# Optimization experiments

Hardware: AMD Instinct MI355X
Metric: run time of the kernel (lower is better)

## Reference

```python
import jax, jax.numpy as jnp
import numpy as np

# Model dims (from init_kwargs)
D_MODEL = 1024
D_STATE = 64
D_CONV = 4
EXPAND = 2
HEADDIM = 128
NGROUPS = 1
D_INNER = EXPAND * D_MODEL              # 2048
NHEADS = D_INNER // HEADDIM             # 16
CONV_DIM = D_INNER + 2 * NGROUPS * D_STATE   # 2176
D_IN_PROJ = 2 * D_INNER + 2 * NGROUPS * D_STATE + NHEADS  # 4240
BATCH, SEQLEN = 2, 2048
DT_MIN, DT_MAX, DT_FLOOR = 1e-3, 1e-1, 1e-4
RMS_EPS = 1e-5


def setup_inputs() -> dict:
    key = jax.random.key(0)
    ks = jax.random.split(key, 8)
    u = jax.random.normal(ks[0], (BATCH, SEQLEN, D_MODEL), jnp.float32)
    in_proj_w = jax.random.normal(ks[1], (D_IN_PROJ, D_MODEL), jnp.float32) * 0.02
    conv_w = jax.random.normal(ks[2], (CONV_DIM, 1, D_CONV), jnp.float32) * 0.2
    conv_b = jax.random.normal(ks[3], (CONV_DIM,), jnp.float32) * 0.02
    # dt_bias init: inverse-softplus of dt ~ LogUniform(dt_min, dt_max)
    dt = jnp.exp(jax.random.uniform(ks[4], (NHEADS,)) * (jnp.log(DT_MAX) - jnp.log(DT_MIN)) + jnp.log(DT_MIN))
    dt = jnp.maximum(dt, DT_FLOOR)
    dt_bias = dt + jnp.log(-jnp.expm1(-dt))
    A_log = jnp.log(jax.random.uniform(ks[5], (NHEADS,), minval=1.0, maxval=16.0))
    D_param = jnp.ones((NHEADS,), jnp.float32)
    norm_w = jnp.ones((D_INNER,), jnp.float32)
    out_proj_w = jax.random.normal(ks[6], (D_MODEL, D_INNER), jnp.float32) * 0.02
    return {"u": u, "in_proj_w": in_proj_w, "conv_w": conv_w, "conv_b": conv_b,
            "dt_bias": dt_bias, "A_log": A_log, "D_param": D_param,
            "norm_w": norm_w, "out_proj_w": out_proj_w}


def _mamba2_forward(u, in_proj_w, conv_w, conv_b, dt_bias, A_log, D_param, norm_w, out_proj_w):
    B, L, _ = u.shape
    zxbcdt = jnp.einsum('bld,ed->ble', u, in_proj_w)  # (B, L, D_IN_PROJ)
    z = zxbcdt[..., :D_INNER]
    xBC = zxbcdt[..., D_INNER:D_INNER + CONV_DIM]
    dt = jax.nn.softplus(zxbcdt[..., D_INNER + CONV_DIM:] + dt_bias)  # (B, L, H)

    # Depthwise causal conv1d + SiLU
    xc = jnp.swapaxes(xBC, 1, 2)  # (B, C, L)
    xc = jax.lax.conv_general_dilated(xc, conv_w, window_strides=(1,),
                                      padding=[(D_CONV - 1, 0)],
                                      feature_group_count=CONV_DIM)
    xc = jax.nn.silu(xc + conv_b[None, :, None])
    xBC = jnp.swapaxes(xc, 1, 2)  # (B, L, C)

    x = xBC[..., :D_INNER].reshape(B, L, NHEADS, HEADDIM)
    Bmat = xBC[..., D_INNER:D_INNER + D_STATE]          # (B, L, N), ngroups=1
    Cmat = xBC[..., D_INNER + D_STATE:]                 # (B, L, N)

    A = -jnp.exp(A_log)  # (H,)

    def step(state, inp):
        dt_t, x_t, B_t, C_t = inp  # (B,H), (B,H,P), (B,N), (B,N)
        dA = jnp.exp(dt_t * A)[:, :, None, None]
        state = state * dA + (dt_t[:, :, None, None] * x_t[:, :, :, None]) * B_t[:, None, None, :]
        y_t = jnp.einsum('bhpn,bn->bhp', state, C_t) + D_param[None, :, None] * x_t
        return state, y_t

    state0 = jnp.zeros((B, NHEADS, HEADDIM, D_STATE), u.dtype)
    inputs = (jnp.moveaxis(dt, 1, 0), jnp.moveaxis(x, 1, 0),
              jnp.moveaxis(Bmat, 1, 0), jnp.moveaxis(Cmat, 1, 0))
    _, ys = jax.lax.scan(step, state0, inputs)
    y = jnp.moveaxis(ys, 0, 1).reshape(B, L, D_INNER)

    # RMSNormGated (norm_before_gate=False): gate first, then normalize
    yg = y * jax.nn.silu(z)
    rms = jax.lax.rsqrt(jnp.mean(yg * yg, axis=-1, keepdims=True) + RMS_EPS)
    yn = yg * rms * norm_w

    return jnp.einsum('ble,de->bld', yn, out_proj_w)


def reference(u, in_proj_w, conv_w, conv_b, dt_bias, A_log, D_param, norm_w, out_proj_w):
    return _mamba2_forward(u, in_proj_w, conv_w, conv_b, dt_bias, A_log, D_param, norm_w, out_proj_w)
```

## Files before the change

kernel.cpp:

```cpp
#include <hip/hip_runtime.h>
#include <cstdint>
#include <cstddef>

#define D_MODEL   1024
#define D_STATE   64
#define D_CONV    4
#define HEADDIM   128
#define NHEADS    16
#define D_INNER   2048
#define CONV_DIM  2176
#define D_IN_PROJ 4240
#define NPAD      4352
#define BATCH     2
#define SEQLEN    2048
#define NROWS     (BATCH*SEQLEN)
#define CHUNK     64
#define NCHUNK    (SEQLEN/CHUNK)

using u16   = unsigned short;
using s16x8 = __attribute__((ext_vector_type(8))) short;
using f32x4 = __attribute__((ext_vector_type(4))) float;

__device__ __forceinline__ u16 f2bf(float f) {
    union { float f; unsigned u; } v; v.f = f;
    unsigned r = v.u + 0x7fffu + ((v.u >> 16) & 1u);
    return (u16)(r >> 16);
}
__device__ __forceinline__ float bf2f(u16 x) {
    union { unsigned u; float f; } v; v.u = ((unsigned)x) << 16;
    return v.f;
}

__device__ __forceinline__ void gload16(const u16* g, u16* l) {
    __builtin_amdgcn_global_load_lds(
        (const __attribute__((address_space(1))) unsigned int*)g,
        (__attribute__((address_space(3))) unsigned int*)l, 16, 0, 0);
}

__device__ __forceinline__ void cp8(const float* in, u16* out, int i) {
    const float4* p = (const float4*)(in + (size_t)i * 8);
    float4 a = p[0], b = p[1];
    u16 o[8] = {f2bf(a.x), f2bf(a.y), f2bf(a.z), f2bf(a.w),
                f2bf(b.x), f2bf(b.y), f2bf(b.z), f2bf(b.w)};
    *(uint4*)(out + (size_t)i * 8) = *(const uint4*)o;
}

#define CVT_N0 (NROWS*D_MODEL/8)
#define CVT_N1 (NPAD*128)
#define CVT_N2 (D_MODEL*D_INNER/8)
__global__ __launch_bounds__(256) void cvt_all(
    const float* __restrict__ u, const float* __restrict__ w_in,
    const float* __restrict__ w_out,
    u16* __restrict__ u_bf, u16* __restrict__ w_in_bf, u16* __restrict__ w_out_bf)
{
    int i = blockIdx.x * 256 + threadIdx.x;
    if (i < CVT_N0) {
        cp8(u, u_bf, i);
    } else if (i < CVT_N0 + CVT_N1) {
        int j = i - CVT_N0;
        int row = j >> 7, seg = j & 127;
        u16 o[8] = {0,0,0,0,0,0,0,0};
        if (row < D_IN_PROJ) {
            const float4* p = (const float4*)(w_in + (size_t)row * D_MODEL + seg * 8);
            float4 a = p[0], b = p[1];
            o[0]=f2bf(a.x); o[1]=f2bf(a.y); o[2]=f2bf(a.z); o[3]=f2bf(a.w);
            o[4]=f2bf(b.x); o[5]=f2bf(b.y); o[6]=f2bf(b.z); o[7]=f2bf(b.w);
        }
        *(uint4*)(w_in_bf + (size_t)j * 8) = *(const uint4*)o;
    } else if (i < CVT_N0 + CVT_N1 + CVT_N2) {
        cp8(w_out, w_out_bf, i - CVT_N0 - CVT_N1);
    }
}

#define CPITCH 136
__global__ __launch_bounds__(512) void gemm_in512(
    const u16* __restrict__ A, const u16* __restrict__ B, int K,
    u16* __restrict__ C0, int n1, int ld0,
    u16* __restrict__ C1, int n2, int ld1,
    u16* __restrict__ C2, int n3, int ld2)
{
    __shared__ u16 smem[4 * 128 * 64];

    const int tid  = threadIdx.x;
    const int wid  = tid >> 6;
    const int lane = tid & 63;
    const int wm   = wid >> 2, wn = wid & 3;

    const int gx   = gridDim.x;
    int orig = blockIdx.y * gx + blockIdx.x;
    const int xcd = orig & 7;
    const int loc = orig >> 3;
    const int mt  = (xcd >> 1) * 8  + (loc & 7);
    const int nt  = (xcd & 1) * 17 + (loc >> 3);
    const int m0 = mt * 128, n0 = nt * 128;

    const int lrow = lane >> 3;
    const int lseg = (lane & 7) ^ lrow;
    const u16* gA = A + (size_t)(m0 + lrow) * K + lseg * 8;
    const u16* gB = B + (size_t)(n0 + lrow) * K + lseg * 8;

    f32x4 acc[4][2];
    #pragma unroll
    for (int i = 0; i < 4; ++i)
        #pragma unroll
        for (int j = 0; j < 2; ++j)
            acc[i][j] = (f32x4){0.f, 0.f, 0.f, 0.f};

    const int fr = lane & 15, fq = lane >> 4;
    const int nstep = K >> 6;

    auto stage = [&](int buf, int k0) {
        u16* sAp = smem + buf * 8192;
        u16* sBp = smem + 16384 + buf * 8192;
        #pragma unroll
        for (int i = 0; i < 2; ++i) {
            const int r0 = (i * 8 + wid) * 8;
            gload16(gA + (size_t)r0 * K + k0, sAp + r0 * 64);
            gload16(gB + (size_t)r0 * K + k0, sBp + r0 * 64);
        }
    };

    stage(0, 0);
    int cur = 0;
    for (int step = 0; step < nstep; ++step) {
        if (step + 1 < nstep) {
            stage(cur ^ 1, (step + 1) * 64);
            asm volatile("s_waitcnt vmcnt(4)" ::: "memory");
        } else {
            asm volatile("s_waitcnt vmcnt(0)" ::: "memory");
        }
        __builtin_amdgcn_s_barrier();
        __builtin_amdgcn_sched_barrier(0);

        const u16* sAc = smem + cur * 8192;
        const u16* sBc = smem + 16384 + cur * 8192;
        #pragma unroll
        for (int ks = 0; ks < 2; ++ks) {
            s16x8 bfr[2];
            #pragma unroll
            for (int ni = 0; ni < 2; ++ni) {
                const int row = wn * 32 + ni * 16 + fr;
                const int bo = row * 128 + ((ks * 64 + fq * 16) ^ ((row & 7) << 4));
                bfr[ni] = *(const s16x8*)((const char*)sBc + bo);
            }
            #pragma unroll
            for (int mi = 0; mi < 4; ++mi) {
                const int row = wm * 64 + mi * 16 + fr;
                const int bo = row * 128 + ((ks * 64 + fq * 16) ^ ((row & 7) << 4));
                s16x8 af = *(const s16x8*)((const char*)sAc + bo);
                #pragma unroll
                for (int ni = 0; ni < 2; ++ni)
                    acc[mi][ni] = __builtin_amdgcn_mfma_f32_16x16x32_bf16(
                        af, bfr[ni], acc[mi][ni], 0, 0, 0);
            }
        }

        __builtin_amdgcn_sched_barrier(0);
        __builtin_amdgcn_s_barrier();
        cur ^= 1;
    }
    __builtin_amdgcn_sched_barrier(0);

    u16* sC = smem;
    #pragma unroll
    for (int mi = 0; mi < 4; ++mi) {
        #pragma unroll
        for (int j = 0; j < 4; ++j) {
            const int rl = wm * 64 + mi * 16 + fq * 4 + j;
            #pragma unroll
            for (int ni = 0; ni < 2; ++ni) {
                const int cl = wn * 32 + ni * 16 + fr;
                sC[rl * CPITCH + cl] = f2bf(acc[mi][ni][j]);
            }
        }
    }
    __syncthreads();
    #pragma unroll
    for (int k2 = 0; k2 < 4; ++k2) {
        const int g  = tid + k2 * 512;
        const int rl = g >> 4, cg = g & 15;
        uint4 v = *(const uint4*)&sC[rl * CPITCH + cg * 8];
        const int r = m0 + rl, c = n0 + cg * 8;
        if (c < n1)      *(uint4*)(C0 + (size_t)r * ld0 + c)        = v;
        else if (c < n2) *(uint4*)(C1 + (size_t)r * ld1 + (c - n1)) = v;
        else if (c < n3) *(uint4*)(C2 + (size_t)r * ld2 + (c - n2)) = v;
    }
}

__global__ __launch_bounds__(512) void gemm_out512(
    const u16* __restrict__ A, const u16* __restrict__ B, int K,
    float* __restrict__ C, int N)
{
    __shared__ u16 smem[4 * 128 * 64];

    const int tid  = threadIdx.x;
    const int wid  = tid >> 6;
    const int lane = tid & 63;
    const int wm   = wid >> 2, wn = wid & 3;

    const int gx   = gridDim.x;
    const int nwg  = gx * gridDim.y;
    const int cpx  = nwg >> 3;
    int orig = blockIdx.y * gx + blockIdx.x;
    int wg   = (orig & 7) * cpx + (orig >> 3);
    const int m0 = (wg / gx) * 128, n0 = (wg % gx) * 128;

    const int lrow = lane >> 3;
    const int lseg = (lane & 7) ^ lrow;
    const u16* gA = A + (size_t)(m0 + lrow) * K + lseg * 8;
    const u16* gB = B + (size_t)(n0 + lrow) * K + lseg * 8;

    f32x4 acc[4][2];
    #pragma unroll
    for (int i = 0; i < 4; ++i)
        #pragma unroll
        for (int j = 0; j < 2; ++j)
            acc[i][j] = (f32x4){0.f, 0.f, 0.f, 0.f};

    const int fr = lane & 15, fq = lane >> 4;
    const int nstep = K >> 6;

    auto stage = [&](int buf, int k0) {
        u16* sAp = smem + buf * 8192;
        u16* sBp = smem + 16384 + buf * 8192;
        #pragma unroll
        for (int i = 0; i < 2; ++i) {
            const int r0 = (i * 8 + wid) * 8;
            gload16(gA + (size_t)r0 * K + k0, sAp + r0 * 64);
            gload16(gB + (size_t)r0 * K + k0, sBp + r0 * 64);
        }
    };

    stage(0, 0);
    int cur = 0;
    for (int step = 0; step < nstep; ++step) {
        if (step + 1 < nstep) {
            stage(cur ^ 1, (step + 1) * 64);
            asm volatile("s_waitcnt vmcnt(4)" ::: "memory");
        } else {
            asm volatile("s_waitcnt vmcnt(0)" ::: "memory");
        }
        __builtin_amdgcn_s_barrier();
        __builtin_amdgcn_sched_barrier(0);

        const u16* sAc = smem + cur * 8192;
        const u16* sBc = smem + 16384 + cur * 8192;
        #pragma unroll
        for (int ks = 0; ks < 2; ++ks) {
            s16x8 bfr[2];
            #pragma unroll
            for (int ni = 0; ni < 2; ++ni) {
                const int row = wn * 32 + ni * 16 + fr;
                const int bo = row * 128 + ((ks * 64 + fq * 16) ^ ((row & 7) << 4));
                bfr[ni] = *(const s16x8*)((const char*)sBc + bo);
            }
            #pragma unroll
            for (int mi = 0; mi < 4; ++mi) {
                const int row = wm * 64 + mi * 16 + fr;
                const int bo = row * 128 + ((ks * 64 + fq * 16) ^ ((row & 7) << 4));
                s16x8 af = *(const s16x8*)((const char*)sAc + bo);
                #pragma unroll
                for (int ni = 0; ni < 2; ++ni)
                    acc[mi][ni] = __builtin_amdgcn_mfma_f32_16x16x32_bf16(
                        af, bfr[ni], acc[mi][ni], 0, 0, 0);
            }
        }

        __builtin_amdgcn_sched_barrier(0);
        __builtin_amdgcn_s_barrier();
        cur ^= 1;
    }
    __builtin_amdgcn_sched_barrier(0);

    float* sCf = (float*)smem;
    #pragma unroll
    for (int h2 = 0; h2 < 2; ++h2) {
        if (wm == h2) {
            #pragma unroll
            for (int mi = 0; mi < 4; ++mi)
                #pragma unroll
                for (int j = 0; j < 4; ++j) {
                    const int rl = mi * 16 + fq * 4 + j;
                    #pragma unroll
                    for (int ni = 0; ni < 2; ++ni) {
                        const int cl = wn * 32 + ni * 16 + fr;
                        sCf[rl * 132 + cl] = acc[mi][ni][j];
                    }
                }
        }
        __syncthreads();
        #pragma unroll
        for (int k2 = 0; k2 < 4; ++k2) {
            const int g  = tid + k2 * 512;
            const int rl = g >> 5, cg = g & 31;
            float4 v = *(const float4*)&sCf[rl * 132 + cg * 4];
            *(float4*)(C + (size_t)(m0 + h2 * 64 + rl) * N + n0 + cg * 4) = v;
        }
        __syncthreads();
    }
}

#define NCONV8 (NROWS*(CONV_DIM/8))
__global__ __launch_bounds__(256) void conv_silu_dt(
    const u16* __restrict__ xBC, const float* __restrict__ conv_w,
    const float* __restrict__ conv_b, u16* __restrict__ xconv,
    const u16* __restrict__ dtraw, const float* __restrict__ dt_bias,
    float* __restrict__ dtw)
{
    int idx = blockIdx.x * 256 + threadIdx.x;
    if (idx < NCONV8) {
        int c8  = idx % (CONV_DIM / 8);
        int row = idx / (CONV_DIM / 8);
        int l   = row % SEQLEN;
        int b   = row / SEQLEN;
        int c0  = c8 * 8;
        const u16* src = xBC + (size_t)(b * SEQLEN) * CONV_DIM + c0;

        uint4 z4 = {0u, 0u, 0u, 0u};
        uint4 v3 = *(const uint4*)(src + (size_t)l * CONV_DIM);
        uint4 v2 = (l >= 1) ? *(const uint4*)(src + (size_t)(l-1) * CONV_DIM) : z4;
        uint4 v1 = (l >= 2) ? *(const uint4*)(src + (size_t)(l-2) * CONV_DIM) : z4;
        uint4 v0 = (l >= 3) ? *(const uint4*)(src + (size_t)(l-3) * CONV_DIM) : z4;
        const u16* p0 = (const u16*)&v0; const u16* p1 = (const u16*)&v1;
        const u16* p2 = (const u16*)&v2; const u16* p3 = (const u16*)&v3;

        u16 o[8];
        #pragma unroll
        for (int j = 0; j < 8; ++j) {
            const float4 w4 = *(const float4*)(conv_w + (size_t)(c0 + j) * 4);
            float acc = conv_b[c0 + j]
                      + bf2f(p0[j]) * w4.x + bf2f(p1[j]) * w4.y
                      + bf2f(p2[j]) * w4.z + bf2f(p3[j]) * w4.w;
            o[j] = f2bf(acc / (1.f + expf(-acc)));
        }
        *(uint4*)(xconv + (size_t)row * CONV_DIM + c0) = *(const uint4*)o;
    } else {
        int k = idx - NCONV8;
        if (k < NROWS * NHEADS) {
            int h = k & (NHEADS - 1);
            float v = bf2f(dtraw[k]) + dt_bias[h];
            dtw[k] = (v > 20.f) ? v : log1pf(expf(v));
        }
    }
}

__global__ __launch_bounds__(256) void chunk_state(
    const u16* __restrict__ xconv, const float* __restrict__ dtw,
    const float* __restrict__ A_log, u16* __restrict__ Sbuf,
    float* __restrict__ Tbuf)
{
    const int blk = blockIdx.x;
    const int k  = blk & (NCHUNK-1);
    const int bh = blk >> 5;
    const int b  = bh >> 4, h = bh & 15;
    const int tid = threadIdx.x;
    const int wid = tid >> 6, lane = tid & 63;
    const float A = -expf(A_log[h]);

    __shared__ float sdt[CHUNK], sW[CHUNK], sT;
    __shared__ u16   sWB16[CHUNK * D_STATE];
    __shared__ u16   sX[CHUNK * HEADDIM];

    const int t0 = k * CHUNK;
    const u16* xc = xconv + (size_t)(b*SEQLEN + t0) * CONV_DIM;

    if (tid < CHUNK)
        sdt[tid] = dtw[(size_t)(b*SEQLEN + t0 + tid)*NHEADS + h];
    __syncthreads();
    if (tid < CHUNK) {
        float a = 0.f, pref = 0.f;
        for (int r = 0; r < CHUNK; ++r) {
            a += sdt[r] * A;
            if (r == tid) pref = a;
        }
        sW[tid] = __expf(a - pref) * sdt[tid];
        if (tid == 0) sT = a;
    }
    __syncthreads();

    #pragma unroll
    for (int c = 0; c < 4; ++c) {
        const int r = wid * 16 + c * 4 + (lane >> 4);
        const int seg = lane & 15;
        gload16(xc + (size_t)r * CONV_DIM + h * HEADDIM + seg * 8,
                sX + (wid * 16 + c * 4) * HEADDIM);
    }
    {
        const int s = tid >> 2, nb = tid & 3;
        const float wv = sW[s];
        uint4 b0 = *(const uint4*)(xc + (size_t)s*CONV_DIM + D_INNER + nb*16);
        uint4 b1 = *(const uint4*)(xc + (size_t)s*CONV_DIM + D_INNER + nb*16 + 8);
        const u16* pb0 = (const u16*)&b0; const u16* pb1 = (const u16*)&b1;
        u16 o[16];
        #pragma unroll
        for (int j = 0; j < 8; ++j) {
            o[j]     = f2bf(wv * bf2f(pb0[j]));
            o[8 + j] = f2bf(wv * bf2f(pb1[j]));
        }
        #pragma unroll
        for (int u2 = 0; u2 < 2; ++u2) {
            const int bo = s * 128 + ((nb * 32 + u2 * 16) ^ ((s & 7) << 4));
            *(uint4*)((char*)sWB16 + bo) = *(const uint4*)&o[u2 * 8];
        }
    }
    __syncthreads();

    const int nn = tid >> 4, pp = tid & 15;
    const int p0 = pp * 8, n0 = nn * 4;
    const int base16 = (nn >> 1) << 4;
    const int sub8   = (nn & 1) * 8;
    float acc[4][8];
    #pragma unroll
    for (int i = 0; i < 4; ++i)
        #pragma unroll
        for (int j = 0; j < 8; ++j) acc[i][j] = 0.f;

    for (int sb = 0; sb < CHUNK; sb += 4) {
        #pragma unroll
        for (int si = 0; si < 4; ++si) {
            const int s = sb + si;
            const int bo = s * 128 + ((base16 ^ ((s & 7) << 4)) + sub8);
            uint2 wv2 = *(const uint2*)((const char*)sWB16 + bo);
            const u16* wp = (const u16*)&wv2;
            const float w0f = bf2f(wp[0]), w1f = bf2f(wp[1]);
            const float w2f = bf2f(wp[2]), w3f = bf2f(wp[3]);
            uint4 xv = *(const uint4*)&sX[s * HEADDIM + p0];
            const u16* xp = (const u16*)&xv;
            #pragma unroll
            for (int j = 0; j < 8; ++j) {
                const float xf = bf2f(xp[j]);
                acc[0][j] += w0f * xf;
                acc[1][j] += w1f * xf;
                acc[2][j] += w2f * xf;
                acc[3][j] += w3f * xf;
            }
        }
    }
    u16* So = Sbuf + ((size_t)bh*NCHUNK + k)*(D_STATE*HEADDIM);
    #pragma unroll
    for (int i = 0; i < 4; ++i) {
        u16 o[8];
        #pragma unroll
        for (int j = 0; j < 8; ++j) o[j] = f2bf(acc[i][j]);
        *(uint4*)(So + (size_t)(n0 + i) * HEADDIM + p0) = *(const uint4*)o;
    }
    if (tid == 0) Tbuf[bh*NCHUNK + k] = sT;
}

__global__ __launch_bounds__(256) void chunk_seq_par(u16* __restrict__ Sbuf,
                                                     const float* __restrict__ Tbuf)
{
    const int blk = blockIdx.x;
    const int bh  = blk >> 3;
    const int sub = blk & 7;
    __shared__ float seT[NCHUNK];
    if (threadIdx.x < NCHUNK)
        seT[threadIdx.x] = __expf(Tbuf[bh*NCHUNK + threadIdx.x]);
    __syncthreads();

    const int idx4 = sub * 256 + threadIdx.x;
    u16* base = Sbuf + (size_t)bh*NCHUNK*(D_STATE*HEADDIM) + (size_t)idx4*4;
    float run[4];
    #pragma unroll
    for (int j = 0; j < 4; ++j) run[j] = 0.f;
    for (int k = 0; k < NCHUNK; ++k) {
        u16* p = base + (size_t)k * (D_STATE*HEADDIM);
        uint2 v = *(const uint2*)p;
        const u16* pv = (const u16*)&v;
        const float eT = seT[k];
        u16 o[4];
        #pragma unroll
        for (int j = 0; j < 4; ++j) {
            float tmp = bf2f(pv[j]);
            o[j] = f2bf(run[j]);
            run[j] = run[j] * eT + tmp;
        }
        *(uint2*)p = *(const uint2*)o;
    }
}

__global__ __launch_bounds__(256) void chunk_output(
    const u16* __restrict__ xconv, const float* __restrict__ dtw,
    const float* __restrict__ A_log, const float* __restrict__ D_param,
    const u16* __restrict__ Sbuf, u16* __restrict__ y)
{
    const int blk = blockIdx.x;
    const int k  = blk & (NCHUNK-1);
    const int bh = blk >> 5;
    const int b  = bh >> 4, h = bh & 15;
    const int tid = threadIdx.x;
    const int wid = tid >> 6, lane = tid & 63;
    const float A  = -expf(A_log[h]);
    const float Dp = D_param[h];

    __shared__ u16 sMt16[(CHUNK + D_STATE) * CHUNK];
    __shared__ u16 sX[CHUNK * HEADDIM];
    float* sdt = (float*)sMt16;
    float* sL  = sdt + CHUNK;

    const int t0 = k * CHUNK;
    const u16* xc = xconv + (size_t)(b*SEQLEN + t0) * CONV_DIM;

    if (tid < CHUNK)
        sdt[tid] = dtw[(size_t)(b*SEQLEN + t0 + tid)*NHEADS + h];
    __syncthreads();
    if (tid < CHUNK) {
        float a = 0.f, pref = 0.f;
        for (int r = 0; r < CHUNK; ++r) {
            a += sdt[r] * A;
            if (r == tid) pref = a;
        }
        sL[tid] = pref;
    }
    __syncthreads();

    #pragma unroll
    for (int c = 0; c < 4; ++c) {
        const int r = wid * 16 + c * 4 + (lane >> 4);
        const int seg = lane & 15;
        gload16(xc + (size_t)r * CONV_DIM + h * HEADDIM + seg * 8,
                sX + (wid * 16 + c * 4) * HEADDIM);
    }

    const int fr = lane & 15, fq = lane >> 4;
    float4 sL4 = *(const float4*)&sL[wid * 16 + fq * 4];
    const float Lt[4] = {sL4.x, sL4.y, sL4.z, sL4.w};
    float pre_L[4], pre_dt[4];
    #pragma unroll
    for (int sf = 0; sf < 4; ++sf) {
        const int s_row = sf * 16 + fr;
        pre_L[sf]  = sL[s_row];
        pre_dt[sf] = sdt[s_row];
    }
    const int tM = tid >> 2, nbM = tid & 3;
    const float elM = __expf(sL[tM]);
    __syncthreads();

    {
        const int t_row = wid * 16 + fr;
        s16x8 cfrag[2];
        #pragma unroll
        for (int ks = 0; ks < 2; ++ks)
            cfrag[ks] = *(const s16x8*)(xc + (size_t)t_row*CONV_DIM + D_INNER + D_STATE
                                        + ks*32 + fq*8);

        #pragma unroll
        for (int sf = 0; sf < 4; ++sf) {
            const int s_row = sf * 16 + fr;
            f32x4 g = (f32x4){0.f, 0.f, 0.f, 0.f};
            #pragma unroll
            for (int ks = 0; ks < 2; ++ks) {
                s16x8 bfrag = *(const s16x8*)(xc + (size_t)s_row*CONV_DIM + D_INNER
                                              + ks*32 + fq*8);
                g = __builtin_amdgcn_mfma_f32_16x16x32_bf16(cfrag[ks], bfrag, g, 0, 0, 0);
            }
            const float Ls  = pre_L[sf];
            const float dts = pre_dt[sf];
            u16 o[4];
            #pragma unroll
            for (int r = 0; r < 4; ++r) {
                const int t = wid * 16 + fq * 4 + r;
                const float e = __expf(fminf(Lt[r] - Ls, 0.f)) * dts;
                o[r] = f2bf((s_row <= t) ? g[r] * e : 0.f);
            }
            const int bo2 = s_row * 128 + ((wid * 32 + fq * 8) ^ ((s_row & 7) << 4));
            *(uint2*)((char*)sMt16 + bo2) = *(const uint2*)o;
        }
    }

    {
        uint4 c0 = *(const uint4*)(xc + (size_t)tM*CONV_DIM + D_INNER + D_STATE + nbM*16);
        uint4 c1 = *(const uint4*)(xc + (size_t)tM*CONV_DIM + D_INNER + D_STATE + nbM*16 + 8);
        const u16* pc0 = (const u16*)&c0; const u16* pc1 = (const u16*)&c1;
        #pragma unroll
        for (int j = 0; j < 16; ++j) {
            const int n = nbM * 16 + j;
            const float v = elM * bf2f(j < 8 ? pc0[j] : pc1[j - 8]);
            const int bo2 = (CHUNK + n) * 128 + ((tM * 2) ^ ((n & 7) << 4));
            *(u16*)((char*)sMt16 + bo2) = f2bf(v);
        }
    }
    __syncthreads();

    const int tt = tid >> 4, pp = tid & 15;
    const int p0 = pp * 8;
    float acc[4][8];
    #pragma unroll
    for (int i = 0; i < 4; ++i)
        #pragma unroll
        for (int j = 0; j < 8; ++j) acc[i][j] = 0.f;

    const int smax = tt * 4 + 4;
    for (int sb = 0; sb < smax; sb += 4) {
        #pragma unroll
        for (int si = 0; si < 4; ++si) {
            const int s = sb + si;
            const int bo = s * 128 + ((tt * 8) ^ ((s & 7) << 4));
            uint2 mv = *(const uint2*)((const char*)sMt16 + bo);
            const u16* mp = (const u16*)&mv;
            const float m0f = bf2f(mp[0]), m1f = bf2f(mp[1]);
            const float m2f = bf2f(mp[2]), m3f = bf2f(mp[3]);
            uint4 xv = *(const uint4*)&sX[s * HEADDIM + p0];
            const u16* xp = (const u16*)&xv;
            #pragma unroll
            for (int j = 0; j < 8; ++j) {
                const float xf = bf2f(xp[j]);
                acc[0][j] += m0f * xf;
                acc[1][j] += m1f * xf;
                acc[2][j] += m2f * xf;
                acc[3][j] += m3f * xf;
            }
        }
    }
    const u16* Sinit = Sbuf + ((size_t)bh*NCHUNK + k)*(D_STATE*HEADDIM);
    #pragma unroll 8
    for (int n = 0; n < D_STATE; ++n) {
        const int bo = (CHUNK + n) * 128 + ((tt * 8) ^ ((n & 7) << 4));
        uint2 mv = *(const uint2*)((const char*)sMt16 + bo);
        const u16* mp = (const u16*)&mv;
        const float m0f = bf2f(mp[0]), m1f = bf2f(mp[1]);
        const float m2f = bf2f(mp[2]), m3f = bf2f(mp[3]);
        uint4 sv = *(const uint4*)(Sinit + (size_t)n * HEADDIM + p0);
        const u16* sp = (const u16*)&sv;
        #pragma unroll
        for (int j = 0; j < 8; ++j) {
            const float sf = bf2f(sp[j]);
            acc[0][j] += m0f * sf;
            acc[1][j] += m1f * sf;
            acc[2][j] += m2f * sf;
            acc[3][j] += m3f * sf;
        }
    }
    #pragma unroll
    for (int i = 0; i < 4; ++i) {
        const int t = tt * 4 + i;
        uint4 xv = *(const uint4*)&sX[t * HEADDIM + p0];
        const u16* xp = (const u16*)&xv;
        u16 o[8];
        #pragma unroll
        for (int j = 0; j < 8; ++j)
            o[j] = f2bf(acc[i][j] + Dp * bf2f(xp[j]));
        *(uint4*)(y + ((size_t)(b*SEQLEN + t0 + t))*D_INNER + h*HEADDIM + p0)
            = *(const uint4*)o;
    }
}

__global__ __launch_bounds__(256) void gate_rmsnorm(const u16* __restrict__ z,
                                                    const u16* __restrict__ y,
                                                    const float* __restrict__ norm_w,
                                                    u16* __restrict__ yn)
{
    const int row = blockIdx.x;
    const int tid = threadIdx.x;
    const u16* zr = z + (size_t)row * D_INNER + tid * 8;
    const u16* yr = y + (size_t)row * D_INNER + tid * 8;
    u16*       o  = yn + (size_t)row * D_INNER + tid * 8;

    uint4 zv4 = *(const uint4*)zr;
    uint4 yv4 = *(const uint4*)yr;
    const u16* zp = (const u16*)&zv4;
    const u16* yp = (const u16*)&yv4;

    float vals[8];
    float ss = 0.f;
    #pragma unroll
    for (int j = 0; j < 8; ++j) {
        float zv = bf2f(zp[j]);
        float g  = bf2f(yp[j]) * (zv / (1.f + expf(-zv)));
        vals[j] = g;
        ss += g * g;
    }
    #pragma unroll
    for (int off = 32; off > 0; off >>= 1) ss += __shfl_down(ss, off);
    __shared__ float red[4];
    __shared__ float sscale;
    int wid = tid >> 6, lane = tid & 63;
    if (lane == 0) red[wid] = ss;
    __syncthreads();
    if (tid == 0)
        sscale = rsqrtf((red[0]+red[1]+red[2]+red[3]) / (float)D_INNER + 1e-5f);
    __syncthreads();
    float rms = sscale;
    const float4* nw = (const float4*)(norm_w + tid * 8);
    float4 w0 = nw[0], w1 = nw[1];
    float wv[8] = {w0.x,w0.y,w0.z,w0.w,w1.x,w1.y,w1.z,w1.w};
    u16 ov[8];
    #pragma unroll
    for (int j = 0; j < 8; ++j) ov[j] = f2bf(vals[j] * rms * wv[j]);
    *(uint4*)o = *(const uint4*)ov;
}

extern "C" void kernel_launch(void* const* d_in, const int* in_sizes, int n_in,
                              void* d_out, int out_size, void* d_ws, size_t ws_size,
                              hipStream_t stream)
{
    const float* u          = (const float*)d_in[0];
    const float* in_proj_w  = (const float*)d_in[1];
    const float* conv_w     = (const float*)d_in[2];
    const float* conv_b     = (const float*)d_in[3];
    const float* dt_bias    = (const float*)d_in[4];
    const float* A_log      = (const float*)d_in[5];
    const float* D_param    = (const float*)d_in[6];
    const float* norm_w     = (const float*)d_in[7];
    const float* out_proj_w = (const float*)d_in[8];
    float* out = (float*)d_out;

    char* w = (char*)d_ws;
    u16* z_bf     = (u16*)w;  w += (size_t)NROWS * D_INNER  * 2;
    u16* xBC_bf   = (u16*)w;  w += (size_t)NROWS * CONV_DIM * 2;
    u16* xconv_bf = (u16*)w;  w += (size_t)NROWS * CONV_DIM * 2;
    u16* yb_bf    = (u16*)w;  w += (size_t)NROWS * D_INNER  * 2;
    u16* dtraw_bf = (u16*)w;  w += (size_t)NROWS * NHEADS   * 2;
    float* dtw    = (float*)w; w += (size_t)NROWS * NHEADS  * 4;
    float* Tbuf   = (float*)w; w += (size_t)BATCH*NHEADS*NCHUNK * 4;
    u16* Sbuf     = (u16*)w;  w += (size_t)BATCH*NHEADS*NCHUNK*D_STATE*HEADDIM * 2;
    u16* u_bf     = (u16*)w;  w += (size_t)NROWS * D_MODEL  * 2;
    u16* w_in_bf  = (u16*)w;  w += (size_t)NPAD  * D_MODEL  * 2;
    u16* w_out_bf = (u16*)w;  w += (size_t)D_MODEL * D_INNER * 2;
    u16* yn_bf    = xconv_bf;

    cvt_all<<<(CVT_N0+CVT_N1+CVT_N2 + 255)/256, 256, 0, stream>>>(
        u, in_proj_w, out_proj_w, u_bf, w_in_bf, w_out_bf);

    dim3 g1(NPAD/128, NROWS/128);
    gemm_in512<<<g1, 512, 0, stream>>>(u_bf, w_in_bf, D_MODEL,
                                       z_bf, D_INNER, D_INNER,
                                       xBC_bf, D_INNER + CONV_DIM, CONV_DIM,
                                       dtraw_bf, D_IN_PROJ, NHEADS);

    int ntot = NCONV8 + NROWS * NHEADS;
    conv_silu_dt<<<(ntot + 255) / 256, 256, 0, stream>>>(
        xBC_bf, conv_w, conv_b, xconv_bf, dtraw_bf, dt_bias, dtw);

    chunk_state<<<BATCH*NHEADS*NCHUNK, 256, 0, stream>>>(xconv_bf, dtw, A_log, Sbuf, Tbuf);
    chunk_seq_par<<<BATCH*NHEADS*8, 256, 0, stream>>>(Sbuf, Tbuf);
    chunk_output<<<BATCH*NHEADS*NCHUNK, 256, 0, stream>>>(xconv_bf, dtw, A_log, D_param,
                                                          Sbuf, yb_bf);

    gate_rmsnorm<<<NROWS, 256, 0, stream>>>(z_bf, yb_bf, norm_w, yn_bf);

    dim3 g6(D_MODEL/128, NROWS/128);
    gemm_out512<<<g6, 512, 0, stream>>>(yn_bf, w_out_bf, D_INNER, out, D_MODEL);
}
```

Before: 202.9 us.

## Use MFMA for chunk output intra-chunk and state contributions

Replaces the scalar FMA loops in chunk_output with bf16 MFMA: the masked decay matrix and scaled C are concatenated into one 64x128 A operand, and x and the initial state are transposed into swizzled LDS as the B operand. Results go through an LDS staging buffer so global stores are coalesced. This cuts the FP32 ALU work of the two GEMM-like loops, at the cost of scattered 2-byte transposing LDS writes and an extra synchronisation. The causal-mask skipping that the scalar loop exploited is lost, so the full 64-wide K range is always computed.

```diff
diff --git a/kernel.cpp b/kernel.cpp
--- a/kernel.cpp
+++ b/kernel.cpp
@@ -493,13 +493,17 @@
     const float A  = -expf(A_log[h]);
     const float Dp = D_param[h];
 
-    __shared__ u16 sMt16[(CHUNK + D_STATE) * CHUNK];
-    __shared__ u16 sX[CHUNK * HEADDIM];
-    float* sdt = (float*)sMt16;
+    __shared__ u16 arena[3 * 8192];
+    u16* Mfull = arena;
+    u16* sXT   = arena + 8192;
+    u16* sST   = arena + 16384;
+    u16* eT    = arena + 8192;
+    float* sdt = (float*)Mfull;
     float* sL  = sdt + CHUNK;
 
     const int t0 = k * CHUNK;
     const u16* xc = xconv + (size_t)(b*SEQLEN + t0) * CONV_DIM;
+    const u16* Sinit = Sbuf + ((size_t)bh*NCHUNK + k)*(D_STATE*HEADDIM);
 
     if (tid < CHUNK)
         sdt[tid] = dtw[(size_t)(b*SEQLEN + t0 + tid)*NHEADS + h];
@@ -514,14 +518,6 @@
     }
     __syncthreads();
 
-    #pragma unroll
-    for (int c = 0; c < 4; ++c) {
-        const int r = wid * 16 + c * 4 + (lane >> 4);
-        const int seg = lane & 15;
-        gload16(xc + (size_t)r * CONV_DIM + h * HEADDIM + seg * 8,
-                sX + (wid * 16 + c * 4) * HEADDIM);
-    }
-
     const int fr = lane & 15, fq = lane >> 4;
     float4 sL4 = *(const float4*)&sL[wid * 16 + fq * 4];
     const float Lt[4] = {sL4.x, sL4.y, sL4.z, sL4.w};
@@ -537,6 +533,28 @@
     __syncthreads();
 
     {
+        const int sr = tid >> 2;
+        const int pg = tid & 3;
+        #pragma unroll
+        for (int i = 0; i < 4; ++i) {
+            const int pb = pg * 32 + i * 8;
+            uint4 xv = *(const uint4*)(xc + (size_t)sr * CONV_DIM + h * HEADDIM + pb);
+            const u16* xp = (const u16*)&xv;
+            uint4 sv = *(const uint4*)(Sinit + (size_t)sr * HEADDIM + pb);
+            const u16* sp = (const u16*)&sv;
+            const int cb = sr * 2;
+            const int cbase = (cb & ~15), coff = (cb & 15);
+            #pragma unroll
+            for (int j = 0; j < 8; ++j) {
+                const int p = pb + j;
+                const int bo = p * 128 + (cbase ^ ((p & 7) << 4)) + coff;
+                *(u16*)((char*)sXT + bo) = xp[j];
+                *(u16*)((char*)sST + bo) = sp[j];
+            }
+        }
+    }
+
+    {
         const int t_row = wid * 16 + fr;
         s16x8 cfrag[2];
         #pragma unroll
@@ -556,92 +574,83 @@
             }
             const float Ls  = pre_L[sf];
             const float dts = pre_dt[sf];
-            u16 o[4];
+            const int cb = s_row * 2;
+            const int cbase = (cb & ~15), coff = (cb & 15);
             #pragma unroll
             for (int r = 0; r < 4; ++r) {
                 const int t = wid * 16 + fq * 4 + r;
                 const float e = __expf(fminf(Lt[r] - Ls, 0.f)) * dts;
-                o[r] = f2bf((s_row <= t) ? g[r] * e : 0.f);
-            }
-            const int bo2 = s_row * 128 + ((wid * 32 + fq * 8) ^ ((s_row & 7) << 4));
-            *(uint2*)((char*)sMt16 + bo2) = *(const uint2*)o;
-        }
-    }
-
+                const float val = (s_row <= t) ? g[r] * e : 0.f;
+                const int bo = t * 256 + (cbase ^ ((t & 7) << 4)) + coff;
+                *(u16*)((char*)Mfull + bo) = f2bf(val);
+            }
+        }
+    }
     {
         uint4 c0 = *(const uint4*)(xc + (size_t)tM*CONV_DIM + D_INNER + D_STATE + nbM*16);
         uint4 c1 = *(const uint4*)(xc + (size_t)tM*CONV_DIM + D_INNER + D_STATE + nbM*16 + 8);
         const u16* pc0 = (const u16*)&c0; const u16* pc1 = (const u16*)&c1;
-        #pragma unroll
-        for (int j = 0; j < 16; ++j) {
-            const int n = nbM * 16 + j;
-            const float v = elM * bf2f(j < 8 ? pc0[j] : pc1[j - 8]);
-            const int bo2 = (CHUNK + n) * 128 + ((tM * 2) ^ ((n & 7) << 4));
-            *(u16*)((char*)sMt16 + bo2) = f2bf(v);
-        }
-    }
-    __syncthreads();
-
-    const int tt = tid >> 4, pp = tid & 15;
-    const int p0 = pp * 8;
-    float acc[4][8];
-    #pragma unroll
-    for (int i = 0; i < 4; ++i)
-        #pragma unroll
-        for (int j = 0; j < 8; ++j) acc[i][j] = 0.f;
-
-    const int smax = tt * 4 + 4;
-    for (int sb = 0; sb < smax; sb += 4) {
-        #pragma unroll
-        for (int si = 0; si < 4; ++si) {
-            const int s = sb + si;
-            const int bo = s * 128 + ((tt * 8) ^ ((s & 7) << 4));
-            uint2 mv = *(const uint2*)((const char*)sMt16 + bo);
-            const u16* mp = (const u16*)&mv;
-            const float m0f = bf2f(mp[0]), m1f = bf2f(mp[1]);
-            const float m2f = bf2f(mp[2]), m3f = bf2f(mp[3]);
-            uint4 xv = *(const uint4*)&sX[s * HEADDIM + p0];
-            const u16* xp = (const u16*)&xv;
-            #pragma unroll
-            for (int j = 0; j < 8; ++j) {
-                const float xf = bf2f(xp[j]);
-                acc[0][j] += m0f * xf;
-                acc[1][j] += m1f * xf;
-                acc[2][j] += m2f * xf;
-                acc[3][j] += m3f * xf;
-            }
-        }
-    }
-    const u16* Sinit = Sbuf + ((size_t)bh*NCHUNK + k)*(D_STATE*HEADDIM);
-    #pragma unroll 8
-    for (int n = 0; n < D_STATE; ++n) {
-        const int bo = (CHUNK + n) * 128 + ((tt * 8) ^ ((n & 7) << 4));
-        uint2 mv = *(const uint2*)((const char*)sMt16 + bo);
-        const u16* mp = (const u16*)&mv;
-        const float m0f = bf2f(mp[0]), m1f = bf2f(mp[1]);
-        const float m2f = bf2f(mp[2]), m3f = bf2f(mp[3]);
-        uint4 sv = *(const uint4*)(Sinit + (size_t)n * HEADDIM + p0);
-        const u16* sp = (const u16*)&sv;
-        #pragma unroll
-        for (int j = 0; j < 8; ++j) {
-            const float sf = bf2f(sp[j]);
-            acc[0][j] += m0f * sf;
-            acc[1][j] += m1f * sf;
-            acc[2][j] += m2f * sf;
-            acc[3][j] += m3f * sf;
-        }
-    }
-    #pragma unroll
-    for (int i = 0; i < 4; ++i) {
-        const int t = tt * 4 + i;
-        uint4 xv = *(const uint4*)&sX[t * HEADDIM + p0];
-        const u16* xp = (const u16*)&xv;
-        u16 o[8];
-        #pragma unroll
-        for (int j = 0; j < 8; ++j)
-            o[j] = f2bf(acc[i][j] + Dp * bf2f(xp[j]));
-        *(uint4*)(y + ((size_t)(b*SEQLEN + t0 + t))*D_INNER + h*HEADDIM + p0)
-            = *(const uint4*)o;
+        u16 o[16];
+        #pragma unroll
+        for (int j = 0; j < 16; ++j)
+            o[j] = f2bf(elM * bf2f(j < 8 ? pc0[j] : pc1[j - 8]));
+        #pragma unroll
+        for (int u2 = 0; u2 < 2; ++u2) {
+            const int cb = 128 + nbM * 32 + u2 * 16;
+            const int bo = tM * 256 + (cb ^ ((tM & 7) << 4));
+            *(uint4*)((char*)Mfull + bo) = *(const uint4*)&o[u2 * 8];
+        }
+    }
+    __syncthreads();
+
+    f32x4 accB[8];
+    #pragma unroll
+    for (int i = 0; i < 8; ++i) accB[i] = (f32x4){0.f, 0.f, 0.f, 0.f};
+
+    #pragma unroll
+    for (int ks = 0; ks < 4; ++ks) {
+        const int ta = wid * 16 + fr;
+        const int boA = ta * 256 + ((ks * 64 + fq * 16) ^ ((ta & 7) << 4));
+        s16x8 afr = *(const s16x8*)((const char*)Mfull + boA);
+        const u16* src = (ks < 2) ? sXT : sST;
+        const int cbB = (ks & 1) * 64 + fq * 16;
+        #pragma unroll
+        for (int pt = 0; pt < 8; ++pt) {
+            const int p = pt * 16 + fr;
+            const int boB = p * 128 + (cbB ^ ((p & 7) << 4));
+            s16x8 bfrB = *(const s16x8*)((const char*)src + boB);
+            accB[pt] = __builtin_amdgcn_mfma_f32_16x16x32_bf16(afr, bfrB, accB[pt], 0, 0, 0);
+        }
+    }
+
+    #pragma unroll
+    for (int pt = 0; pt < 8; ++pt) {
+        const int p = pt * 16 + fr;
+        #pragma unroll
+        for (int r = 0; r < 4; ++r) {
+            const int t = wid * 16 + fq * 4 + r;
+            const int cb = t * 2;
+            const int bo = p * 128 + ((cb & ~15) ^ ((p & 7) << 4)) + (cb & 15);
+            accB[pt][r] += Dp * bf2f(*(const u16*)((const char*)sXT + bo));
+        }
+    }
+    __syncthreads();
+
+    #pragma unroll
+    for (int pt = 0; pt < 8; ++pt) {
+        #pragma unroll
+        for (int r = 0; r < 4; ++r) {
+            const int t = wid * 16 + fq * 4 + r;
+            eT[t * CPITCH + pt * 16 + fr] = f2bf(accB[pt][r]);
+        }
+    }
+    __syncthreads();
+    #pragma unroll
+    for (int k2 = 0; k2 < 4; ++k2) {
+        const int g  = tid + k2 * 256;
+        const int rl = g >> 4, cg = g & 15;
+        uint4 v = *(const uint4*)&eT[rl * CPITCH + cg * 8];
+        *(uint4*)(y + ((size_t)(b*SEQLEN + t0 + rl))*D_INNER + h*HEADDIM + cg*8) = v;
     }
 }
 
```

After: 181.9 us. -10.3%, faster.
